# Kernel tuning notes

Hardware: AMD Instinct MI355X
Metric: run time of the kernel (lower is better)

## Reference

```python
import jax, jax.numpy as jnp
import numpy as np

EPS = 1e-6
H = 16; D_NOPE = 128; D_ROPE = 64; D_V = 128; D_QK = D_NOPE + D_ROPE
Q_RANK = 1536; KV_RANK = 512; HID = 2048


def rmsnorm(x, w):
    var = jnp.mean(jnp.square(x.astype(jnp.float32)), axis=-1, keepdims=True)
    return (x * jax.lax.rsqrt(var + EPS)).astype(x.dtype) * w


def rotate_half(x):
    x1, x2 = jnp.split(x, 2, axis=-1)
    return jnp.concatenate([-x2, x1], axis=-1)


def interleave(x):
    # deepseek interleaved rope: pairs (0,1),(2,3).. -> [evens | odds]
    b, h, s, d = x.shape
    return x.reshape(b, h, s, d // 2, 2).transpose(0, 1, 2, 4, 3).reshape(b, h, s, d)


def setup_inputs() -> dict:
    key = jax.random.key(0)
    ks = jax.random.split(key, 8)
    B, S = 2, 2048
    sc = lambda n: 1.0 / np.sqrt(n)
    inp = {
        'hidden_states': jax.random.normal(ks[0], (B, S, HID), jnp.float32),
        'w_qa': jax.random.normal(ks[1], (HID, Q_RANK), jnp.float32) * sc(HID),
        'g_qa': jnp.ones((Q_RANK,), jnp.float32),
        'w_qb': jax.random.normal(ks[2], (Q_RANK, H * D_QK), jnp.float32) * sc(Q_RANK),
        'w_kva': jax.random.normal(ks[3], (HID, KV_RANK + D_ROPE), jnp.float32) * sc(HID),
        'g_kva': jnp.ones((KV_RANK,), jnp.float32),
        'w_kvb': jax.random.normal(ks[4], (KV_RANK, H * (D_NOPE + D_V)), jnp.float32) * sc(KV_RANK),
        'w_o': jax.random.normal(ks[5], (H * D_V, HID), jnp.float32) * sc(H * D_V),
    }
    pos = jnp.arange(S, dtype=jnp.float32)
    inv = 1.0 / (10000.0 ** (jnp.arange(0, D_ROPE, 2, dtype=jnp.float32) / D_ROPE))
    emb = jnp.concatenate([pos[:, None] * inv[None, :]] * 2, axis=-1)  # [S, 64]
    inp['cos'] = jnp.broadcast_to(jnp.cos(emb)[None], (B, S, D_ROPE))
    inp['sin'] = jnp.broadcast_to(jnp.sin(emb)[None], (B, S, D_ROPE))
    return inp


def reference(hidden_states, w_qa, g_qa, w_qb, w_kva, g_kva, w_kvb, w_o, cos, sin):
    B, S, _ = hidden_states.shape
    scaling = D_QK ** -0.5
    # low-rank Q: q_b_proj(q_a_layernorm(q_a_proj(h)))
    q = rmsnorm(hidden_states @ w_qa, g_qa) @ w_qb
    q = q.reshape(B, S, H, D_QK).transpose(0, 2, 1, 3)          # [B,H,S,192]
    q_pass, q_rot = q[..., :D_NOPE], q[..., D_NOPE:]
    # compressed KV latent + shared rope key
    ckv = hidden_states @ w_kva                                  # [B,S,576]
    k_pass, k_rot = ckv[..., :KV_RANK], ckv[..., KV_RANK:]
    kv = rmsnorm(k_pass, g_kva) @ w_kvb                          # [B,S,H*256]
    kv = kv.reshape(B, S, H, D_NOPE + D_V).transpose(0, 2, 1, 3)
    k_nope, v = kv[..., :D_NOPE], kv[..., D_NOPE:]
    k_rot = k_rot.reshape(B, 1, S, D_ROPE)
    c = cos[:, None, :, :]; sn = sin[:, None, :, :]
    q_rot = interleave(q_rot); k_rot = interleave(k_rot)
    q_rot = q_rot * c + rotate_half(q_rot) * sn
    k_rot = k_rot * c + rotate_half(k_rot) * sn
    k_rot = jnp.broadcast_to(k_rot, (B, H, S, D_ROPE))
    qf = jnp.concatenate([q_pass, q_rot], axis=-1)               # [B,H,S,192]
    kf = jnp.concatenate([k_nope, k_rot], axis=-1)               # [B,H,S,192]
    scores = jnp.einsum('bhqd,bhkd->bhqk', qf, kf) * scaling
    mask = jnp.triu(jnp.full((S, S), jnp.finfo(jnp.float32).min, jnp.float32), 1)
    probs = jax.nn.softmax(scores.astype(jnp.float32) + mask, axis=-1).astype(qf.dtype)
    out = jnp.einsum('bhqk,bhkd->bhqd', probs, v)                # [B,H,S,128]
    out = out.transpose(0, 2, 1, 3).reshape(B, S, H * D_V)
    return out @ w_o
```

## Files before the change

kernel.cpp:

```cpp
#include <hip/hip_runtime.h>

#define DI __device__ __forceinline__

typedef __attribute__((ext_vector_type(8))) unsigned short u16x8;
typedef __attribute__((ext_vector_type(8))) __bf16 bf16x8;
typedef __attribute__((ext_vector_type(4))) float f32x4;

constexpr int B_ = 2, S_ = 2048, H_ = 16, HID_ = 2048;
constexpr int QR = 1536, KVR = 512, DQK = 192;
constexpr int BS = B_ * S_;
constexpr float SCALE = 0.07216878364870323f;
constexpr float QS = SCALE * 1.4426950408889634f;

DI unsigned short f2bf(float x){
  unsigned r;
  asm("v_cvt_pk_bf16_f32 %0, %1, %2" : "=v"(r) : "v"(x), "v"(x));
  return (unsigned short)r;
}
DI float bf2f(unsigned short h){
  return __builtin_bit_cast(float, ((unsigned)h) << 16);
}
DI f32x4 mfma16(u16x8 a, u16x8 b, f32x4 c){
  return __builtin_amdgcn_mfma_f32_16x16x32_bf16(
      __builtin_bit_cast(bf16x8, a), __builtin_bit_cast(bf16x8, b), c, 0, 0, 0);
}
DI void async16(const void* g, void* l){
  __builtin_amdgcn_global_load_lds(
      (__attribute__((address_space(1))) void*)(g),
      (__attribute__((address_space(3))) void*)(l), 16, 0, 0);
}

__global__ __launch_bounds__(256) void cvt_f32_bf16(const float* __restrict__ in,
                                                    unsigned short* __restrict__ out, int n8){
  const int i = blockIdx.x * 256 + threadIdx.x;
  if (i >= n8) return;
  const float4* pp = (const float4*)in + (long)i * 2;
  float4 a = pp[0], b = pp[1];
  u16x8 r;
  r[0]=f2bf(a.x); r[1]=f2bf(a.y); r[2]=f2bf(a.z); r[3]=f2bf(a.w);
  r[4]=f2bf(b.x); r[5]=f2bf(b.y); r[6]=f2bf(b.z); r[7]=f2bf(b.w);
  *(u16x8*)(out + (long)i * 8) = r;
}

__global__ __launch_bounds__(256) void wtrans(const float* __restrict__ W,
                                              unsigned short* __restrict__ Wt,
                                              int K, int N, int Np){
  __shared__ float t[32][33];
  const int n0 = blockIdx.x * 32, k0 = blockIdx.y * 32;
  const int tid = threadIdx.x;
  const int c = tid & 31, r0 = tid >> 5;
  #pragma unroll
  for (int i = 0; i < 4; ++i){
    const int r = r0 + i * 8;
    float v = 0.f;
    if (n0 + c < N) v = W[(long)(k0 + r) * N + n0 + c];
    t[r][c] = v;
  }
  __syncthreads();
  #pragma unroll
  for (int i = 0; i < 4; ++i){
    const int r = r0 + i * 8;
    Wt[(long)(n0 + r) * K + k0 + c] = f2bf(t[c][r]);
  }
}

template<int COLS>
__global__ __launch_bounds__(256) void rmsnorm_k(const float* __restrict__ X, int ldx,
                                                 const float* __restrict__ g,
                                                 unsigned short* __restrict__ Y, int ldy){
  constexpr int PT = COLS / 256;
  const int row = blockIdx.x, tid = threadIdx.x;
  const float* xr = X + (long)row * ldx;
  float v[PT];
  float ss = 0.f;
  #pragma unroll
  for (int i = 0; i < PT; ++i){ v[i] = xr[tid + i * 256]; ss += v[i] * v[i]; }
  #pragma unroll
  for (int off = 32; off >= 1; off >>= 1) ss += __shfl_xor(ss, off);
  __shared__ float red[4];
  if ((tid & 63) == 0) red[tid >> 6] = ss;
  __syncthreads();
  const float tot = red[0] + red[1] + red[2] + red[3];
  const float rs = rsqrtf(tot / (float)COLS + 1e-6f);
  #pragma unroll
  for (int i = 0; i < PT; ++i)
    Y[(long)row * ldy + tid + i * 256] = f2bf(v[i] * rs * g[tid + i * 256]);
}

__global__ __launch_bounds__(256) void gemm_bt(const unsigned short* __restrict__ A,
                                               const unsigned short* __restrict__ Bt,
                                               float* __restrict__ C, int N, int K){
  __shared__ unsigned short lA[128 * 64];
  __shared__ unsigned short lB[128 * 64];
  const int tid = threadIdx.x;
  const int w = tid >> 6, lane = tid & 63, lr = lane & 15, lg = lane >> 4;
  const int wm = w >> 1, wn = w & 1;
  const long m0 = (long)blockIdx.y * 128, n0 = (long)blockIdx.x * 128;
  f32x4 acc[4][4] = {};
  const unsigned short* Ab = A + m0 * K;
  const unsigned short* Bb = Bt + n0 * K;
  for (int k0 = 0; k0 < K; k0 += 64){
    #pragma unroll
    for (int s2 = 0; s2 < 4; ++s2){
      const int c = s2 * 256 + tid;
      async16(Ab + (long)(c >> 3) * K + k0 + (c & 7) * 8, &lA[(s2 * 256 + w * 64) * 8]);
      async16(Bb + (long)(c >> 3) * K + k0 + (c & 7) * 8, &lB[(s2 * 256 + w * 64) * 8]);
    }
    __syncthreads();
    u16x8 a[2][4], b[2][4];
    #pragma unroll
    for (int kk = 0; kk < 2; ++kk){
      #pragma unroll
      for (int m = 0; m < 4; ++m)
        a[kk][m] = *(const u16x8*)&lA[(wm * 64 + m * 16 + lr) * 64 + kk * 32 + lg * 8];
      #pragma unroll
      for (int n = 0; n < 4; ++n)
        b[kk][n] = *(const u16x8*)&lB[(wn * 64 + n * 16 + lr) * 64 + kk * 32 + lg * 8];
    }
    #pragma unroll
    for (int kk = 0; kk < 2; ++kk)
      #pragma unroll
      for (int m = 0; m < 4; ++m)
        #pragma unroll
        for (int n = 0; n < 4; ++n)
          acc[m][n] = mfma16(a[kk][m], b[kk][n], acc[m][n]);
    __syncthreads();
  }
  #pragma unroll
  for (int m = 0; m < 4; ++m){
    const long row = m0 + wm * 64 + m * 16 + lg * 4;
    #pragma unroll
    for (int n = 0; n < 4; ++n){
      const long col = n0 + wn * 64 + n * 16 + lr;
      #pragma unroll
      for (int r = 0; r < 4; ++r)
        C[(row + r) * N + col] = acc[m][n][r];
    }
  }
}

__global__ __launch_bounds__(256) void gemm_qpack(const unsigned short* __restrict__ A,
                                                  const unsigned short* __restrict__ Bt,
                                                  const float* __restrict__ cosb,
                                                  const float* __restrict__ sinb,
                                                  unsigned short* __restrict__ qf, int K){
  const int N = 3072;
  __shared__ unsigned short lA[128 * 64];
  __shared__ unsigned short lB[128 * 64];
  const int tid = threadIdx.x;
  const int w = tid >> 6, lane = tid & 63, lr = lane & 15, lg = lane >> 4;
  const int wm = w >> 1, wn = w & 1;
  const long m0 = (long)blockIdx.y * 128, n0 = (long)blockIdx.x * 128;
  f32x4 acc[4][4] = {};
  const unsigned short* Ab = A + m0 * K;
  const unsigned short* Bb = Bt + n0 * K;
  for (int k0 = 0; k0 < K; k0 += 64){
    #pragma unroll
    for (int s2 = 0; s2 < 4; ++s2){
      const int c = s2 * 256 + tid;
      async16(Ab + (long)(c >> 3) * K + k0 + (c & 7) * 8, &lA[(s2 * 256 + w * 64) * 8]);
      async16(Bb + (long)(c >> 3) * K + k0 + (c & 7) * 8, &lB[(s2 * 256 + w * 64) * 8]);
    }
    __syncthreads();
    u16x8 a[2][4], b[2][4];
    #pragma unroll
    for (int kk = 0; kk < 2; ++kk){
      #pragma unroll
      for (int m = 0; m < 4; ++m)
        a[kk][m] = *(const u16x8*)&lA[(wm * 64 + m * 16 + lr) * 64 + kk * 32 + lg * 8];
      #pragma unroll
      for (int n = 0; n < 4; ++n)
        b[kk][n] = *(const u16x8*)&lB[(wn * 64 + n * 16 + lr) * 64 + kk * 32 + lg * 8];
    }
    #pragma unroll
    for (int kk = 0; kk < 2; ++kk)
      #pragma unroll
      for (int m = 0; m < 4; ++m)
        #pragma unroll
        for (int n = 0; n < 4; ++n)
          acc[m][n] = mfma16(a[kk][m], b[kk][n], acc[m][n]);
    __syncthreads();
  }
  #pragma unroll
  for (int m = 0; m < 4; ++m){
    const int rowg = (int)m0 + wm * 64 + m * 16 + lg * 4;
    #pragma unroll
    for (int n = 0; n < 4; ++n){
      const int col = (int)n0 + wn * 64 + n * 16 + lr;
      const int h = (unsigned)col / 192u;
      const int d = col - h * 192;
      #pragma unroll
      for (int r = 0; r < 4; ++r){
        const int rowi = rowg + r;
        const float a = acc[m][n][r];
        const float partner = __shfl_xor(a, 1);
        float val; int dout;
        if (d < 128){ val = a; dout = d; }
        else {
          const int ii = (d - 128) >> 1;
          const float c  = cosb[(long)rowi * 64 + ii];
          const float sn = sinb[(long)rowi * 64 + ii];
          val  = (d & 1) ? (a * c + partner * sn) : (a * c - partner * sn);
          dout = 128 + ((d & 1) << 5) + ii;
        }
        const int b = rowi >> 11, s = rowi & 2047;
        qf[((long)(b * 16 + h) * S_ + s) * DQK + dout] = f2bf(val * QS);
      }
    }
  }
}

__global__ __launch_bounds__(256) void gemm_kvpack(const unsigned short* __restrict__ A,
                                                   const unsigned short* __restrict__ Bt,
                                                   unsigned short* __restrict__ kf,
                                                   unsigned short* __restrict__ kvm, int K){
  const int N = 4096;
  __shared__ unsigned short lA[128 * 64];
  __shared__ unsigned short lB[128 * 64];
  const int tid = threadIdx.x;
  const int w = tid >> 6, lane = tid & 63, lr = lane & 15, lg = lane >> 4;
  const int wm = w >> 1, wn = w & 1;
  const long m0 = (long)blockIdx.y * 128, n0 = (long)blockIdx.x * 128;
  f32x4 acc[4][4] = {};
  const unsigned short* Ab = A + m0 * K;
  const unsigned short* Bb = Bt + n0 * K;
  for (int k0 = 0; k0 < K; k0 += 64){
    #pragma unroll
    for (int s2 = 0; s2 < 4; ++s2){
      const int c = s2 * 256 + tid;
      async16(Ab + (long)(c >> 3) * K + k0 + (c & 7) * 8, &lA[(s2 * 256 + w * 64) * 8]);
      async16(Bb + (long)(c >> 3) * K + k0 + (c & 7) * 8, &lB[(s2 * 256 + w * 64) * 8]);
    }
    __syncthreads();
    u16x8 a[2][4], b[2][4];
    #pragma unroll
    for (int kk = 0; kk < 2; ++kk){
      #pragma unroll
      for (int m = 0; m < 4; ++m)
        a[kk][m] = *(const u16x8*)&lA[(wm * 64 + m * 16 + lr) * 64 + kk * 32 + lg * 8];
      #pragma unroll
      for (int n = 0; n < 4; ++n)
        b[kk][n] = *(const u16x8*)&lB[(wn * 64 + n * 16 + lr) * 64 + kk * 32 + lg * 8];
    }
    #pragma unroll
    for (int kk = 0; kk < 2; ++kk)
      #pragma unroll
      for (int m = 0; m < 4; ++m)
        #pragma unroll
        for (int n = 0; n < 4; ++n)
          acc[m][n] = mfma16(a[kk][m], b[kk][n], acc[m][n]);
    __syncthreads();
  }
  #pragma unroll
  for (int m = 0; m < 4; ++m){
    const int rowg = (int)m0 + wm * 64 + m * 16 + lg * 4;
    #pragma unroll
    for (int n = 0; n < 4; ++n){
      const int col = (int)n0 + wn * 64 + n * 16 + lr;
      const int h = col >> 8, d = col & 255;
      #pragma unroll
      for (int r = 0; r < 4; ++r){
        const int rowi = rowg + r;
        const unsigned short v = f2bf(acc[m][n][r]);
        const int b = rowi >> 11, s = rowi & 2047;
        if (d < 128) kf[((long)(b * 16 + h) * S_ + s) * DQK + d] = v;
        else         kvm[(long)rowi * 4096 + col] = v;
      }
    }
  }
}

__global__ __launch_bounds__(256) void pack_krot(const float* __restrict__ ckv,
                                                 const float* __restrict__ cosb,
                                                 const float* __restrict__ sinb,
                                                 unsigned short* __restrict__ kf){
  const int row = blockIdx.x, tid = threadIdx.x;
  const int b = row >> 11, s = row & 2047;
  const float* cv = ckv + (long)row * 640 + 512;
  const float* cr = cosb + (long)row * 64;
  const float* sr = sinb + (long)row * 64;
  #pragma unroll
  for (int j = 0; j < 4; ++j){
    const int o = j * 256 + tid;
    const int h = o >> 6, i = o & 63, ii = i & 31;
    const float e = cv[2 * ii], od = cv[2 * ii + 1];
    const float c = cr[ii], sn = sr[ii];
    const float val = (i < 32) ? (e * c - od * sn) : (od * c + e * sn);
    kf[((long)(b * 16 + h) * S_ + s) * DQK + 128 + i] = f2bf(val);
  }
}

__global__ __launch_bounds__(256) void pack_v(const unsigned short* __restrict__ kvm,
                                              unsigned short* __restrict__ vt){
  const int bh = blockIdx.x, s0 = blockIdx.y * 64;
  const int b = bh >> 4, h = bh & 15;
  __shared__ unsigned short t[64][130];
  #pragma unroll
  for (int it = 0; it < 32; ++it){
    const int idx = it * 256 + threadIdx.x;
    const int sl = idx >> 7, d = idx & 127;
    t[sl][d] = kvm[(long)(b * S_ + s0 + sl) * 4096 + h * 256 + 128 + d];
  }
  __syncthreads();
  #pragma unroll
  for (int it = 0; it < 32; ++it){
    const int idx = it * 256 + threadIdx.x;
    const int dr = idx >> 6, sc = idx & 63;
    vt[(long)(bh * 128 + dr) * S_ + s0 + sc] = t[sc][dr];
  }
}

__global__ __launch_bounds__(256) void mla_attn(const unsigned short* __restrict__ qf,
                                                const unsigned short* __restrict__ kf,
                                                const unsigned short* __restrict__ vt,
                                                unsigned short* __restrict__ ao){
  __shared__ unsigned short k_lds[64 * 192];
  __shared__ unsigned short v_lds[128 * 64];
  __shared__ unsigned short p_lds[4][32][72];
  const int bid = blockIdx.x;
  const int u = bid >> 5;
  const int qt = (u < 8) ? u : 23 - u;
  const int bh = bid & 31;
  const int b = bh >> 4, h = bh & 15;
  const int tid = threadIdx.x;
  const int w = tid >> 6, lane = tid & 63, lr = lane & 15, lg = lane >> 4;
  const int q0 = qt * 128 + w * 32;
  const unsigned short* qb = qf + (long)bh * S_ * DQK;
  const unsigned short* kb = kf + (long)bh * S_ * DQK;
  const unsigned short* vb = vt + (long)bh * 128 * S_;
  u16x8 aq[2][6];
  #pragma unroll
  for (int mi = 0; mi < 2; ++mi)
    #pragma unroll
    for (int kk = 0; kk < 6; ++kk)
      aq[mi][kk] = *(const u16x8*)&qb[(long)(q0 + mi * 16 + lr) * DQK + kk * 32 + lg * 8];
  f32x4 oacc[2][8] = {};
  f32x4 lacc[2] = {};
  float mrun[2][4];
  #pragma unroll
  for (int mi = 0; mi < 2; ++mi)
    #pragma unroll
    for (int r = 0; r < 4; ++r) mrun[mi][r] = -1e30f;
  u16x8 onesv;
  #pragma unroll
  for (int i = 0; i < 8; ++i) onesv[i] = 0x3F80;
  const int ktiles = (qt + 1) * 2;
  const int myktiles = ((q0 + 31) >> 6) + 1;
  for (int kt = 0; kt < ktiles; ++kt){
    #pragma unroll
    for (int s2 = 0; s2 < 6; ++s2){
      const int c = s2 * 256 + tid;
      const int row = c / 24, col = c - row * 24;
      async16(kb + (long)(kt * 64 + row) * DQK + ((col ^ (row & 7)) << 3),
              &k_lds[(s2 * 256 + w * 64) * 8]);
    }
    #pragma unroll
    for (int s2 = 0; s2 < 4; ++s2){
      const int c = s2 * 256 + tid;
      const int row = c >> 3, col = c & 7;
      async16(vb + (long)row * S_ + kt * 64 + ((col ^ (row & 7)) << 3),
              &v_lds[(s2 * 256 + w * 64) * 8]);
    }
    __syncthreads();
    if (kt < myktiles){
      f32x4 sacc[2][4] = {};
      #pragma unroll
      for (int ni = 0; ni < 4; ++ni){
        const int rowk = ni * 16 + lr;
        #pragma unroll
        for (int kk = 0; kk < 6; ++kk){
          const int col16 = kk * 4 + lg;
          const u16x8 bk = *(const u16x8*)&k_lds[rowk * 192 + ((col16 ^ (rowk & 7)) << 3)];
          sacc[0][ni] = mfma16(aq[0][kk], bk, sacc[0][ni]);
          sacc[1][ni] = mfma16(aq[1][kk], bk, sacc[1][ni]);
        }
      }
      const int kbase = kt * 64;
      if (kbase + 63 > q0){
        #pragma unroll
        for (int mi = 0; mi < 2; ++mi)
          #pragma unroll
          for (int r = 0; r < 4; ++r){
            const int qrow = q0 + mi * 16 + lg * 4 + r;
            #pragma unroll
            for (int ni = 0; ni < 4; ++ni)
              if (kbase + ni * 16 + lr > qrow) sacc[mi][ni][r] = -1e30f;
          }
      }
      #pragma unroll
      for (int mi = 0; mi < 2; ++mi)
        #pragma unroll
        for (int r = 0; r < 4; ++r){
          float tm = fmaxf(fmaxf(sacc[mi][0][r], sacc[mi][1][r]),
                           fmaxf(sacc[mi][2][r], sacc[mi][3][r]));
          tm = fmaxf(tm, __shfl_xor(tm, 1));
          tm = fmaxf(tm, __shfl_xor(tm, 2));
          tm = fmaxf(tm, __shfl_xor(tm, 4));
          tm = fmaxf(tm, __shfl_xor(tm, 8));
          if (tm > mrun[mi][r] + 8.f){
            const float sc = __builtin_exp2f(mrun[mi][r] - tm);
            mrun[mi][r] = tm;
            lacc[mi][r] *= sc;
            #pragma unroll
            for (int d = 0; d < 8; ++d) oacc[mi][d][r] *= sc;
          }
          const float m_ = mrun[mi][r];
          const int qq = mi * 16 + lg * 4 + r;
          p_lds[w][qq][lr]      = f2bf(__builtin_exp2f(sacc[mi][0][r] - m_));
          p_lds[w][qq][16 + lr] = f2bf(__builtin_exp2f(sacc[mi][1][r] - m_));
          p_lds[w][qq][32 + lr] = f2bf(__builtin_exp2f(sacc[mi][2][r] - m_));
          p_lds[w][qq][48 + lr] = f2bf(__builtin_exp2f(sacc[mi][3][r] - m_));
        }
      u16x8 pa[2][2];
      #pragma unroll
      for (int mi = 0; mi < 2; ++mi)
        #pragma unroll
        for (int kk2 = 0; kk2 < 2; ++kk2)
          pa[mi][kk2] = *(const u16x8*)&p_lds[w][mi * 16 + lr][kk2 * 32 + lg * 8];
      #pragma unroll
      for (int mi = 0; mi < 2; ++mi)
        #pragma unroll
        for (int kk2 = 0; kk2 < 2; ++kk2)
          lacc[mi] = mfma16(pa[mi][kk2], onesv, lacc[mi]);
      #pragma unroll
      for (int d = 0; d < 8; ++d){
        const int rowv = d * 16 + lr;
        #pragma unroll
        for (int kk2 = 0; kk2 < 2; ++kk2){
          const int col16 = kk2 * 4 + lg;
          const u16x8 bv = *(const u16x8*)&v_lds[rowv * 64 + ((col16 ^ (rowv & 7)) << 3)];
          oacc[0][d] = mfma16(pa[0][kk2], bv, oacc[0][d]);
          oacc[1][d] = mfma16(pa[1][kk2], bv, oacc[1][d]);
        }
      }
    }
    __syncthreads();
  }
  #pragma unroll
  for (int mi = 0; mi < 2; ++mi)
    #pragma unroll
    for (int r = 0; r < 4; ++r){
      const long row = q0 + mi * 16 + lg * 4 + r;
      const float inv = 1.0f / lacc[mi][r];
      #pragma unroll
      for (int d = 0; d < 8; ++d)
        ao[(long)(b * S_ + row) * 2048 + h * 128 + d * 16 + lr] = f2bf(oacc[mi][d][r] * inv);
    }
}

extern "C" void kernel_launch(void* const* d_in, const int* in_sizes, int n_in,
                              void* d_out, int out_size, void* d_ws, size_t ws_size,
                              hipStream_t stream){
  const float* hid   = (const float*)d_in[0];
  const float* w_qa  = (const float*)d_in[1];
  const float* g_qa  = (const float*)d_in[2];
  const float* w_qb  = (const float*)d_in[3];
  const float* w_kva = (const float*)d_in[4];
  const float* g_kva = (const float*)d_in[5];
  const float* w_kvb = (const float*)d_in[6];
  const float* w_o   = (const float*)d_in[7];
  const float* cosb  = (const float*)d_in[8];
  const float* sinb  = (const float*)d_in[9];
  float* out = (float*)d_out;

  char* p = (char*)d_ws;
  auto alloc = [&](size_t bytes) -> void* {
    void* r = p;
    p += (bytes + 255) & ~(size_t)255;
    return r;
  };
  unsigned short* hb     = (unsigned short*)alloc((size_t)BS * HID_ * 2);
  unsigned short* wqa_t  = (unsigned short*)alloc((size_t)QR * HID_ * 2);
  unsigned short* wqb_t  = (unsigned short*)alloc((size_t)3072 * QR * 2);
  unsigned short* wkva_t = (unsigned short*)alloc((size_t)640 * HID_ * 2);
  unsigned short* wkvb_t = (unsigned short*)alloc((size_t)4096 * KVR * 2);
  unsigned short* wo_t   = (unsigned short*)alloc((size_t)2048 * 2048 * 2);
  float*          qa_f   = (float*)alloc((size_t)BS * QR * 4);
  unsigned short* qan    = (unsigned short*)alloc((size_t)BS * QR * 2);
  float*          ckv_f  = (float*)alloc((size_t)BS * 640 * 4);
  unsigned short* kvn    = (unsigned short*)alloc((size_t)BS * KVR * 2);
  unsigned short* kvmat  = (unsigned short*)alloc((size_t)BS * 4096 * 2);
  unsigned short* qfb    = (unsigned short*)alloc((size_t)32 * S_ * DQK * 2);
  unsigned short* kfb    = (unsigned short*)alloc((size_t)32 * S_ * DQK * 2);
  unsigned short* vtb    = (unsigned short*)alloc((size_t)32 * 128 * S_ * 2);
  unsigned short* aob    = (unsigned short*)alloc((size_t)BS * 2048 * 2);
  (void)ws_size; (void)in_sizes; (void)n_in; (void)out_size;

  cvt_f32_bf16<<<BS * HID_ / 8 / 256, 256, 0, stream>>>(hid, hb, BS * HID_ / 8);
  wtrans<<<dim3(1536 / 32, 2048 / 32), 256, 0, stream>>>(w_qa, wqa_t, 2048, 1536, 1536);
  wtrans<<<dim3(3072 / 32, 1536 / 32), 256, 0, stream>>>(w_qb, wqb_t, 1536, 3072, 3072);
  wtrans<<<dim3(640 / 32, 2048 / 32), 256, 0, stream>>>(w_kva, wkva_t, 2048, 576, 640);
  wtrans<<<dim3(4096 / 32, 512 / 32), 256, 0, stream>>>(w_kvb, wkvb_t, 512, 4096, 4096);
  wtrans<<<dim3(2048 / 32, 2048 / 32), 256, 0, stream>>>(w_o, wo_t, 2048, 2048, 2048);

  gemm_bt<<<dim3(1536 / 128, BS / 128), 256, 0, stream>>>(hb, wqa_t, qa_f, 1536, 2048);
  gemm_bt<<<dim3(640 / 128, BS / 128), 256, 0, stream>>>(hb, wkva_t, ckv_f, 640, 2048);
  rmsnorm_k<1536><<<BS, 256, 0, stream>>>(qa_f, 1536, g_qa, qan, 1536);
  rmsnorm_k<512><<<BS, 256, 0, stream>>>(ckv_f, 640, g_kva, kvn, 512);

  gemm_qpack<<<dim3(3072 / 128, BS / 128), 256, 0, stream>>>(qan, wqb_t, cosb, sinb, qfb, 1536);
  gemm_kvpack<<<dim3(4096 / 128, BS / 128), 256, 0, stream>>>(kvn, wkvb_t, kfb, kvmat, 512);
  pack_krot<<<BS, 256, 0, stream>>>(ckv_f, cosb, sinb, kfb);
  pack_v<<<dim3(32, S_ / 64), 256, 0, stream>>>(kvmat, vtb);

  mla_attn<<<512, 256, 0, stream>>>(qfb, kfb, vtb, aob);

  gemm_bt<<<dim3(2048 / 128, BS / 128), 256, 0, stream>>>(aob, wo_t, out, 2048, 2048);
}
```

Measured before the change: 609.2 us.

## Double-buffer attention K/V tiles, merge q_a/kv_a GEMMs, reorder causal tiles

The attention kernel now double-buffers its K and V LDS tiles: the async load of tile kt+1 is issued before tile kt is computed, so global loads overlap MFMA work. The q_a and kv_a projection weights are packed side by side so a single GEMM (2176 columns) replaces two launches, with rmsnorm and the rope packer reading at offsets into the shared output. Query tiles are scheduled heaviest first to balance the causal workload. The cost is twice the K/V LDS footprint, which may lower occupancy. The merged weight buffer depends on wtrans writing each weight's padding region correctly.

```diff
diff --git a/kernel.cpp b/kernel.cpp
--- a/kernel.cpp
+++ b/kernel.cpp
@@ -11,6 +11,7 @@
 constexpr int BS = B_ * S_;
 constexpr float SCALE = 0.07216878364870323f;
 constexpr float QS = SCALE * 1.4426950408889634f;
+constexpr int CKV_LD = 2176;
 
 DI unsigned short f2bf(float x){
   unsigned r;
@@ -276,7 +277,7 @@
                                                  unsigned short* __restrict__ kf){
   const int row = blockIdx.x, tid = threadIdx.x;
   const int b = row >> 11, s = row & 2047;
-  const float* cv = ckv + (long)row * 640 + 512;
+  const float* cv = ckv + (long)row * CKV_LD + QR + KVR;
   const float* cr = cosb + (long)row * 64;
   const float* sr = sinb + (long)row * 64;
   #pragma unroll
@@ -314,12 +315,12 @@
                                                 const unsigned short* __restrict__ kf,
                                                 const unsigned short* __restrict__ vt,
                                                 unsigned short* __restrict__ ao){
-  __shared__ unsigned short k_lds[64 * 192];
-  __shared__ unsigned short v_lds[128 * 64];
+  __shared__ unsigned short k_lds[2][64 * 192];
+  __shared__ unsigned short v_lds[2][128 * 64];
   __shared__ unsigned short p_lds[4][32][72];
   const int bid = blockIdx.x;
   const int u = bid >> 5;
-  const int qt = (u < 8) ? u : 23 - u;
+  const int qt = (u < 8) ? (15 - u) : (u - 8);
   const int bh = bid & 31;
   const int b = bh >> 4, h = bh & 15;
   const int tid = threadIdx.x;
@@ -346,22 +347,29 @@
   for (int i = 0; i < 8; ++i) onesv[i] = 0x3F80;
   const int ktiles = (qt + 1) * 2;
   const int myktiles = ((q0 + 31) >> 6) + 1;
-  for (int kt = 0; kt < ktiles; ++kt){
+
+  auto stage = [&](int kt, int buf){
     #pragma unroll
     for (int s2 = 0; s2 < 6; ++s2){
       const int c = s2 * 256 + tid;
       const int row = c / 24, col = c - row * 24;
       async16(kb + (long)(kt * 64 + row) * DQK + ((col ^ (row & 7)) << 3),
-              &k_lds[(s2 * 256 + w * 64) * 8]);
+              &k_lds[buf][(s2 * 256 + w * 64) * 8]);
     }
     #pragma unroll
     for (int s2 = 0; s2 < 4; ++s2){
       const int c = s2 * 256 + tid;
       const int row = c >> 3, col = c & 7;
       async16(vb + (long)row * S_ + kt * 64 + ((col ^ (row & 7)) << 3),
-              &v_lds[(s2 * 256 + w * 64) * 8]);
-    }
-    __syncthreads();
+              &v_lds[buf][(s2 * 256 + w * 64) * 8]);
+    }
+  };
+
+  stage(0, 0);
+  __syncthreads();
+  int cur = 0;
+  for (int kt = 0; kt < ktiles; ++kt){
+    if (kt + 1 < ktiles) stage(kt + 1, cur ^ 1);
     if (kt < myktiles){
       f32x4 sacc[2][4] = {};
       #pragma unroll
@@ -370,7 +378,7 @@
         #pragma unroll
         for (int kk = 0; kk < 6; ++kk){
           const int col16 = kk * 4 + lg;
-          const u16x8 bk = *(const u16x8*)&k_lds[rowk * 192 + ((col16 ^ (rowk & 7)) << 3)];
+          const u16x8 bk = *(const u16x8*)&k_lds[cur][rowk * 192 + ((col16 ^ (rowk & 7)) << 3)];
           sacc[0][ni] = mfma16(aq[0][kk], bk, sacc[0][ni]);
           sacc[1][ni] = mfma16(aq[1][kk], bk, sacc[1][ni]);
         }
@@ -428,13 +436,14 @@
         #pragma unroll
         for (int kk2 = 0; kk2 < 2; ++kk2){
           const int col16 = kk2 * 4 + lg;
-          const u16x8 bv = *(const u16x8*)&v_lds[rowv * 64 + ((col16 ^ (rowv & 7)) << 3)];
+          const u16x8 bv = *(const u16x8*)&v_lds[cur][rowv * 64 + ((col16 ^ (rowv & 7)) << 3)];
           oacc[0][d] = mfma16(pa[0][kk2], bv, oacc[0][d]);
           oacc[1][d] = mfma16(pa[1][kk2], bv, oacc[1][d]);
         }
       }
     }
     __syncthreads();
+    cur ^= 1;
   }
   #pragma unroll
   for (int mi = 0; mi < 2; ++mi)
@@ -469,15 +478,15 @@
     p += (bytes + 255) & ~(size_t)255;
     return r;
   };
-  unsigned short* hb     = (unsigned short*)alloc((size_t)BS * HID_ * 2);
-  unsigned short* wqa_t  = (unsigned short*)alloc((size_t)QR * HID_ * 2);
+  unsigned short* hb      = (unsigned short*)alloc((size_t)BS * HID_ * 2);
+  unsigned short* wqakv_t = (unsigned short*)alloc((size_t)CKV_LD * HID_ * 2);
+  unsigned short* wqa_t   = wqakv_t;
+  unsigned short* wkva_t  = wqakv_t + (size_t)QR * HID_;
   unsigned short* wqb_t  = (unsigned short*)alloc((size_t)3072 * QR * 2);
-  unsigned short* wkva_t = (unsigned short*)alloc((size_t)640 * HID_ * 2);
   unsigned short* wkvb_t = (unsigned short*)alloc((size_t)4096 * KVR * 2);
   unsigned short* wo_t   = (unsigned short*)alloc((size_t)2048 * 2048 * 2);
-  float*          qa_f   = (float*)alloc((size_t)BS * QR * 4);
+  float*          qakv_f = (float*)alloc((size_t)BS * CKV_LD * 4);
   unsigned short* qan    = (unsigned short*)alloc((size_t)BS * QR * 2);
-  float*          ckv_f  = (float*)alloc((size_t)BS * 640 * 4);
   unsigned short* kvn    = (unsigned short*)alloc((size_t)BS * KVR * 2);
   unsigned short* kvmat  = (unsigned short*)alloc((size_t)BS * 4096 * 2);
   unsigned short* qfb    = (unsigned short*)alloc((size_t)32 * S_ * DQK * 2);
@@ -493,14 +502,13 @@
   wtrans<<<dim3(4096 / 32, 512 / 32), 256, 0, stream>>>(w_kvb, wkvb_t, 512, 4096, 4096);
   wtrans<<<dim3(2048 / 32, 2048 / 32), 256, 0, stream>>>(w_o, wo_t, 2048, 2048, 2048);
 
-  gemm_bt<<<dim3(1536 / 128, BS / 128), 256, 0, stream>>>(hb, wqa_t, qa_f, 1536, 2048);
-  gemm_bt<<<dim3(640 / 128, BS / 128), 256, 0, stream>>>(hb, wkva_t, ckv_f, 640, 2048);
-  rmsnorm_k<1536><<<BS, 256, 0, stream>>>(qa_f, 1536, g_qa, qan, 1536);
-  rmsnorm_k<512><<<BS, 256, 0, stream>>>(ckv_f, 640, g_kva, kvn, 512);
+  gemm_bt<<<dim3(CKV_LD / 128, BS / 128), 256, 0, stream>>>(hb, wqakv_t, qakv_f, CKV_LD, 2048);
+  rmsnorm_k<1536><<<BS, 256, 0, stream>>>(qakv_f, CKV_LD, g_qa, qan, 1536);
+  rmsnorm_k<512><<<BS, 256, 0, stream>>>(qakv_f + QR, CKV_LD, g_kva, kvn, 512);
 
   gemm_qpack<<<dim3(3072 / 128, BS / 128), 256, 0, stream>>>(qan, wqb_t, cosb, sinb, qfb, 1536);
   gemm_kvpack<<<dim3(4096 / 128, BS / 128), 256, 0, stream>>>(kvn, wkvb_t, kfb, kvmat, 512);
-  pack_krot<<<BS, 256, 0, stream>>>(ckv_f, cosb, sinb, kfb);
+  pack_krot<<<BS, 256, 0, stream>>>(qakv_f, cosb, sinb, kfb);
   pack_v<<<dim3(32, S_ / 64), 256, 0, stream>>>(kvmat, vtb);
 
   mla_attn<<<512, 256, 0, stream>>>(qfb, kfb, vtb, aob);
```

Result: slower. 637.6 us (+4.7%).
